# Optimization experiments

Hardware: AMD Instinct MI355X
Metric: run time of the kernel (lower is better)

The kernel has to match this reference:

```python
import jax, jax.numpy as jnp
import numpy as np

K = 16
EPS = 1e-5
SLOPE = 0.01  # nn.LeakyReLU default


def _bn(x, g, b):
    # BatchNorm1d in training mode applied to [N, C, k] in torch == normalize
    # per-channel over (N, k) axes of [N, k, C] here. Biased variance (ddof=0).
    m = x.mean(axis=(0, 1))
    v = x.var(axis=(0, 1))
    return (x - m) * jax.lax.rsqrt(v + EPS) * g + b


def _lrelu(x):
    return jnp.where(x >= 0, x, SLOPE * x)


def setup_inputs() -> dict:
    key = jax.random.key(0)
    ks = jax.random.split(key, 24)
    N, CIN, COUT = 8192, 256, 256
    s = 0.05
    inp = {
        "fea_i": jax.random.normal(ks[0], (N, CIN), jnp.float32),
        "fea_last": jax.random.normal(ks[1], (N, CIN), jnp.float32),
        "xyz_i": jax.random.uniform(ks[2], (N, 3), jnp.float32),
        "xyz_last": jax.random.uniform(ks[3], (N, 3), jnp.float32),
        "t_i": jnp.float32(2.0),
        "t_last": jnp.float32(1.0),
        # lin_p: Linear(4,64) -> BN(64) -> LeakyReLU -> Linear(64,COUT)
        "wp1": jax.random.normal(ks[4], (4, 64), jnp.float32) * s,
        "bp1": jnp.zeros((64,), jnp.float32),
        "gp": jnp.ones((64,), jnp.float32),
        "bp": jnp.zeros((64,), jnp.float32),
        "wp2": jax.random.normal(ks[5], (64, COUT), jnp.float32) * s,
        "bp2": jnp.zeros((COUT,), jnp.float32),
        # lin_q / lin_k / lin_v
        "wq": jax.random.normal(ks[6], (CIN, COUT), jnp.float32) * s,
        "bq": jnp.zeros((COUT,), jnp.float32),
        "wk": jax.random.normal(ks[7], (CIN, COUT), jnp.float32) * s,
        "bk": jnp.zeros((COUT,), jnp.float32),
        "wv": jax.random.normal(ks[8], (CIN, COUT), jnp.float32) * s,
        "bv": jnp.zeros((COUT,), jnp.float32),
        # lin_w: BN -> LeakyReLU -> Linear(COUT,COUT) -> BN -> LeakyReLU
        "gw1": jnp.ones((COUT,), jnp.float32),
        "bw1": jnp.zeros((COUT,), jnp.float32),
        "ww": jax.random.normal(ks[9], (COUT, COUT), jnp.float32) * s,
        "bw": jnp.zeros((COUT,), jnp.float32),
        "gw2": jnp.ones((COUT,), jnp.float32),
        "bw2": jnp.zeros((COUT,), jnp.float32),
    }
    return inp


def reference(fea_i, fea_last, xyz_i, xyz_last, t_i, t_last,
              wp1, bp1, gp, bp, wp2, bp2,
              wq, bq, wk, bk, wv, bv,
              gw1, bw1, ww, bw, gw2, bw2):
    # k-NN: for each query point in xyz_last, K nearest points in xyz_i
    d2 = (jnp.sum(xyz_last * xyz_last, -1)[:, None]
          + jnp.sum(xyz_i * xyz_i, -1)[None, :]
          - 2.0 * xyz_last @ xyz_i.T)              # [N, N]
    idx = jax.lax.top_k(-d2, K)[1]                 # [N, K] neighbor idx into xyz_i

    fi = fea_i[idx]                                # [N, K, CIN]
    xi = xyz_i[idx]                                # [N, K, 3]
    # pe = xyzt_i - xyzt_last ; the gathered "last" side is the query point itself
    pe = jnp.concatenate([xi - xyz_last[:, None, :],
                          (t_i - t_last) * jnp.ones_like(xi[..., :1])], axis=-1)  # [N,K,4]
    pe = pe @ wp1 + bp1
    pe = _lrelu(_bn(pe, gp, bp))
    pe = pe @ wp2 + bp2                            # [N, K, COUT]

    q = fea_last @ wq + bq                         # [N, COUT], broadcast over K
    w = q[:, None, :] - (fi @ wk + bk) + pe        # [N, K, COUT]
    w = _lrelu(_bn(w, gw1, bw1))
    w = w @ ww + bw
    w = _lrelu(_bn(w, gw2, bw2))
    w = jax.nn.softmax(w, axis=1)                  # softmax over K neighbors

    v = fi @ wv + bv + pe                          # [N, K, COUT]
    return jnp.sum(w * v, axis=1)                  # [N, COUT]
```

## Files before the change

kernel.cpp:

```cpp
#include <hip/hip_runtime.h>
#include <hip/hip_bf16.h>
#include <math.h>

#define N     8192
#define KNN   16
#define NK    (N*KNN)
#define C     256
#define CH    64
#define EPS   1e-5f
#define SLOPE 0.01f
#define LISTMAX 512

typedef __hip_bfloat16 bf16;
typedef short bfrag __attribute__((ext_vector_type(8)));
typedef float ffrag __attribute__((ext_vector_type(4)));

__device__ __forceinline__ float b2f(bf16 x){ return __bfloat162float(x); }
__device__ __forceinline__ bf16  f2b(float x){ return __float2bfloat16(x); }
__device__ __forceinline__ float b2fu(unsigned short s){
    return __uint_as_float(((unsigned)s) << 16);
}
__device__ __forceinline__ unsigned short f2bu(float x){
    union { bf16 h; unsigned short s; } u; u.h = f2b(x); return u.s;
}

union BF8 { unsigned short s[8]; uint4 u; };

template<typename T> __device__ __forceinline__ float ldv(const void* p, int i);
template<> __device__ __forceinline__ float ldv<float>(const void* p, int i){
    return ((const float*)p)[i];
}
template<> __device__ __forceinline__ float ldv<bf16>(const void* p, int i){
    return __bfloat162float(((const bf16*)p)[i]);
}
__device__ __forceinline__ bool is_f32(const void* ti){
    return ((const unsigned short*)ti)[0] == 0;
}

template<typename T>
__device__ __forceinline__ void stage8(const void* src, size_t off,
                                       unsigned short* dst){
    if (sizeof(T) == 4){
        const float4* s = (const float4*)((const float*)src + off);
        float4 a = s[0], b = s[1];
        BF8 o;
        o.s[0]=f2bu(a.x); o.s[1]=f2bu(a.y); o.s[2]=f2bu(a.z); o.s[3]=f2bu(a.w);
        o.s[4]=f2bu(b.x); o.s[5]=f2bu(b.y); o.s[6]=f2bu(b.z); o.s[7]=f2bu(b.w);
        *(uint4*)dst = o.u;
    } else {
        *(uint4*)dst = *(const uint4*)((const unsigned short*)src + off);
    }
}

__device__ __forceinline__ int mbcnt64(unsigned long long b){
    return __builtin_amdgcn_mbcnt_hi((unsigned)(b>>32),
           __builtin_amdgcn_mbcnt_lo((unsigned)b, 0));
}
__device__ __forceinline__ unsigned d2key(float d2){
    unsigned u = __float_as_uint(d2);
    return u ^ (((unsigned)(((int)u) >> 31)) | 0x80000000u);
}

__device__ __align__(256) int    g_idx[NK];
__device__ __align__(256) float  g_S[4096];
__device__ __align__(256) float  g_Rep[4*64*256];
__device__ __align__(256) float  g_M2[2048*9];
__device__ __align__(256) float4 g_pts[N];
__device__ __align__(256) int    g_cellCnt[4096];
__device__ __align__(256) int    g_cellStart[4100];
__device__ __align__(256) int    g_cellCur[4096];
__device__ __align__(256) float4 g_spts[N];
__device__ __align__(256) int    g_sidx[N];
__device__ __align__(256) unsigned short g_qT [C*C];
__device__ __align__(256) unsigned short g_kT [C*C];
__device__ __align__(256) unsigned short g_vT [C*C];
__device__ __align__(256) unsigned short g_wwT[C*C];
__device__ __align__(256) unsigned short g_p2T[C*CH];
__device__ __align__(256) unsigned short g_q  [N*C];
__device__ __align__(256) unsigned short g_fkb[N*C];
__device__ __align__(256) unsigned short g_fvb[N*C];
__device__ __align__(256) bf16   g_w1[NK*C];
__device__ __align__(256) bf16   g_vv[NK*C];
__device__ __align__(256) bf16   g_w2[NK*C];

__device__ __forceinline__ int cell_of(float4 c){
    int cx = (int)(c.x*16.f); cx = cx<0?0:(cx>15?15:cx);
    int cy = (int)(c.y*16.f); cy = cy<0?0:(cy>15?15:cy);
    int cz = (int)(c.z*16.f); cz = cz<0?0:(cz>15?15:cz);
    return (cz<<8) | (cy<<4) | cx;
}

__global__ __launch_bounds__(256) void kprepall(const void* xyz_i,
        const void* wq, const void* wk, const void* wv, const void* ww,
        const void* wp2, const void* ti_){
#pragma clang fp contract(off)
    const int b = blockIdx.x, tid = threadIdx.x;
    const bool f = is_f32(ti_);
    if (b < 64){
        int i = b*256 + tid;
        #pragma unroll
        for (int k = 0; k < 4; k++) g_Rep[i*4 + k] = 0.f;
        if (b < 16) g_S[i] = 0.f;
        else if (b < 32) g_cellCnt[(b-16)*256 + tid] = 0;
    } else if (b < 96){
        int p = (b-64)*256 + tid;
        float x = f ? ldv<float>(xyz_i, p*3+0) : ldv<bf16>(xyz_i, p*3+0);
        float y = f ? ldv<float>(xyz_i, p*3+1) : ldv<bf16>(xyz_i, p*3+1);
        float z = f ? ldv<float>(xyz_i, p*3+2) : ldv<bf16>(xyz_i, p*3+2);
        g_pts[p] = make_float4(x, y, z, (x*x + y*y) + z*z);
    } else {
        const void* src; unsigned short* dst; int K; int i0;
        if      (b <  352){ src=wq;  dst=g_qT;  K=256; i0=(b-  96)*256; }
        else if (b <  608){ src=wk;  dst=g_kT;  K=256; i0=(b- 352)*256; }
        else if (b <  864){ src=wv;  dst=g_vT;  K=256; i0=(b- 608)*256; }
        else if (b < 1120){ src=ww;  dst=g_wwT; K=256; i0=(b- 864)*256; }
        else              { src=wp2; dst=g_p2T; K=64;  i0=(b-1120)*256; }
        int i = i0 + tid;
        int k = i >> 8, n = i & 255;
        float v = f ? ldv<float>(src, i) : ldv<bf16>(src, i);
        dst[n*K + k] = f2bu(v);
    }
}

__global__ __launch_bounds__(256) void khist(){
    int p = blockIdx.x*256 + threadIdx.x;
    atomicAdd(&g_cellCnt[cell_of(g_pts[p])], 1);
}
__global__ __launch_bounds__(256) void kscan(){
    __shared__ int sc[256];
    const int tid = threadIdx.x;
    int carry = 0;
    for (int ch = 0; ch < 16; ch++){
        int i = ch*256 + tid;
        int v = g_cellCnt[i];
        sc[tid] = v;
        __syncthreads();
        for (int s = 1; s < 256; s <<= 1){
            int t_ = (tid >= s) ? sc[tid - s] : 0;
            __syncthreads();
            sc[tid] += t_;
            __syncthreads();
        }
        int excl = carry + sc[tid] - v;
        g_cellStart[i] = excl;
        g_cellCur[i]   = excl;
        carry += sc[255];
        __syncthreads();
    }
    if (tid == 0) g_cellStart[4096] = carry;
}
__global__ __launch_bounds__(256) void kscatter(){
    int p = blockIdx.x*256 + threadIdx.x;
    float4 c = g_pts[p];
    int pos = atomicAdd(&g_cellCur[cell_of(c)], 1);
    g_spts[pos] = c;
    g_sidx[pos] = p;
}

template<int D>
__device__ unsigned sel16(float qx, float qy, float qz, float sq, int lane){
#pragma clang fp contract(off)
    unsigned kk[D];
    #pragma unroll
    for (int i = 0; i < D; i++) kk[i] = 0xFFFFFFFFu;
    for (int t = 0; t < N/64; t++){
        float4 c = g_pts[t*64 + lane];
        float dot = (qx*c.x + qy*c.y) + qz*c.z;
        float d2  = (sq + c.w) - 2.0f*dot;
        unsigned u = d2key(d2);
        #pragma unroll
        for (int j = D-1; j > 0; --j){
            unsigned hi = (kk[j-1] > u) ? kk[j-1] : u;
            kk[j] = (kk[j] < hi) ? kk[j] : hi;
        }
        kk[0] = (kk[0] < u) ? kk[0] : u;
    }
    unsigned v16 = 0;
    for (int it = 0; it < 16; ++it){
        unsigned m = kk[0];
        #pragma unroll
        for (int s = 1; s < 64; s <<= 1){
            unsigned o = (unsigned)__shfl_xor((int)m, s, 64);
            m = (m < o) ? m : o;
        }
        unsigned long long ball = __ballot(kk[0] == m);
        int w = __ffsll(ball) - 1;
        if (lane == w){
            #pragma unroll
            for (int j = 0; j < D-1; j++) kk[j] = kk[j+1];
            kk[D-1] = 0xFFFFFFFFu;
        }
        v16 = m;
    }
    return v16;
}

__device__ int2 scan16(float qx, float qy, float qz, float sq, unsigned v16,
                       int lane, int* sure, int* tie){
#pragma clang fp contract(off)
    int nsure = 0, ntie = 0;
    for (int t = 0; t < N/64; t++){
        const int p = t*64 + lane;
        float4 c = g_pts[p];
        float dot = (qx*c.x + qy*c.y) + qz*c.z;
        float d2  = (sq + c.w) - 2.0f*dot;
        unsigned u = d2key(d2);
        bool bs = (u < v16), bt = (u == v16);
        unsigned long long Bs = __ballot(bs);
        unsigned long long Bt = __ballot(bt);
        if (bs){
            int pos = nsure + mbcnt64(Bs);
            if (pos < 16) sure[pos] = p;
        }
        if (bt){
            int pos = ntie + mbcnt64(Bt);
            if (pos < 16) tie[pos] = p;
        }
        nsure += (int)__popcll(Bs);
        ntie  += (int)__popcll(Bt);
    }
    return make_int2(nsure, ntie);
}

template<typename T>
__device__ void kknn_body(const void* xyz_last, int* sureL, int* tieL,
                          int* listL, float* momL){
#pragma clang fp contract(off)
    const int lane  = threadIdx.x & 63;
    const int wslot = threadIdx.x >> 6;
    const int q     = (blockIdx.x*256 + threadIdx.x) >> 6;
    const float qx = ldv<T>(xyz_last, q*3+0);
    const float qy = ldv<T>(xyz_last, q*3+1);
    const float qz = ldv<T>(xyz_last, q*3+2);
    const float sq = (qx*qx + qy*qy) + qz*qz;
    int* sure = &sureL[wslot*16];
    int* tie  = &tieL [wslot*16];
    int* list = &listL[wslot*LISTMAX];

    int cqx = (int)(qx*16.f); cqx = cqx<0?0:(cqx>15?15:cqx);
    int cqy = (int)(qy*16.f); cqy = cqy<0?0:(cqy>15?15:cqy);
    int cqz = (int)(qz*16.f); cqz = cqz<0?0:(cqz>15?15:cqz);

    int cnt0 = 0, cnt1 = 0, cs0 = 0, cs1 = 0;
    #pragma unroll
    for (int h = 0; h < 2; h++){
        int idx = lane*2 + h;
        if (idx < 125){
            int iz = idx/25, r = idx - iz*25, iy = r/5, ix = r - iy*5;
            int cx = cqx+ix-2, cy = cqy+iy-2, cz = cqz+iz-2;
            if ((unsigned)cx < 16u && (unsigned)cy < 16u && (unsigned)cz < 16u){
                int cell = (cz<<8) | (cy<<4) | cx;
                int s = g_cellStart[cell], e = g_cellStart[cell+1];
                if (h == 0){ cs0 = s; cnt0 = e - s; }
                else       { cs1 = s; cnt1 = e - s; }
            }
        }
    }
    int tot = cnt0 + cnt1;
    int incl = tot;
    #pragma unroll
    for (int s = 1; s < 64; s <<= 1){
        int u = __shfl_up(incl, s, 64);
        if (lane >= s) incl += u;
    }
    const int Tn = __shfl(incl, 63, 64);
    int base = incl - tot;
    bool full = (Tn > LISTMAX) || (Tn < 16);
    unsigned v16 = 0;
    int nsure = 0, ntie = 0;
    if (!full){
        for (int i = 0; i < cnt0; i++) list[base+i] = cs0 + i;
        for (int i = 0; i < cnt1; i++) list[base+cnt0+i] = cs1 + i;
        unsigned kk[4] = {~0u,~0u,~0u,~0u};
        int chunks = (Tn + 63) >> 6;
        for (int t = 0; t < chunks; t++){
            int li = t*64 + lane;
            unsigned u = 0xFFFFFFFFu;
            if (li < Tn){
                float4 c = g_spts[list[li]];
                float dot = (qx*c.x + qy*c.y) + qz*c.z;
                u = d2key((sq + c.w) - 2.0f*dot);
            }
            #pragma unroll
            for (int j = 3; j > 0; --j){
                unsigned hi = (kk[j-1] > u) ? kk[j-1] : u;
                kk[j] = (kk[j] < hi) ? kk[j] : hi;
            }
            kk[0] = (kk[0] < u) ? kk[0] : u;
        }
        for (int it = 0; it < 16; ++it){
            unsigned m = kk[0];
            #pragma unroll
            for (int s = 1; s < 64; s <<= 1){
                unsigned o = (unsigned)__shfl_xor((int)m, s, 64);
                m = (m < o) ? m : o;
            }
            unsigned long long ball = __ballot(kk[0] == m);
            int w = __ffsll(ball) - 1;
            if (lane == w){
                kk[0]=kk[1]; kk[1]=kk[2]; kk[2]=kk[3]; kk[3]=0xFFFFFFFFu;
            }
            v16 = m;
        }
        const float h_ = 0.0625f;
        float dmin = 1e30f;
        if (cqx-2 > 0)  dmin = fminf(dmin, qx - (float)(cqx-2)*h_);
        if (cqx+3 < 16) dmin = fminf(dmin, (float)(cqx+3)*h_ - qx);
        if (cqy-2 > 0)  dmin = fminf(dmin, qy - (float)(cqy-2)*h_);
        if (cqy+3 < 16) dmin = fminf(dmin, (float)(cqy+3)*h_ - qy);
        if (cqz-2 > 0)  dmin = fminf(dmin, qz - (float)(cqz-2)*h_);
        if (cqz+3 < 16) dmin = fminf(dmin, (float)(cqz+3)*h_ - qz);
        unsigned ub = d2key(dmin*dmin);
        if (!(v16 < ub)) full = true;
    }
    if (!full){
        int chunks = (Tn + 63) >> 6;
        for (int t = 0; t < chunks; t++){
            int li = t*64 + lane;
            unsigned u = 0xFFFFFFFFu; int oi = 0;
            if (li < Tn){
                int pos = list[li];
                float4 c = g_spts[pos];
                oi = g_sidx[pos];
                float dot = (qx*c.x + qy*c.y) + qz*c.z;
                u = d2key((sq + c.w) - 2.0f*dot);
            }
            bool bs = (li < Tn) && (u < v16);
            bool bt = (li < Tn) && (u == v16);
            unsigned long long Bs = __ballot(bs);
            unsigned long long Bt = __ballot(bt);
            if (bs){
                int pos2 = nsure + mbcnt64(Bs);
                if (pos2 < 16) sure[pos2] = oi;
            }
            if (bt){
                int pos2 = ntie + mbcnt64(Bt);
                if (pos2 < 16) tie[pos2] = oi;
            }
            nsure += (int)__popcll(Bs);
            ntie  += (int)__popcll(Bt);
        }
        if (nsure > 16 || (ntie > 16 && nsure < 16)) full = true;
    }
    const bool gridok = !full;
    if (full){
        v16 = sel16<16>(qx, qy, qz, sq, lane);
        int2 c2 = scan16(qx, qy, qz, sq, v16, lane, sure, tie);
        nsure = c2.x; ntie = c2.y;
    }
    if (nsure > 16) nsure = 16;
    int vsel = 0;
    if (lane < 16 && lane < nsure) vsel = sure[lane];
    if (gridok){
        int tv = (lane < (ntie < 16 ? ntie : 16)) ? tie[lane] : 0x7FFFFFFF;
        #pragma unroll
        for (int k = 2; k <= 16; k <<= 1)
            #pragma unroll
            for (int j = k>>1; j > 0; j >>= 1){
                int o = __shfl_xor(tv, j, 64);
                bool asc = ((lane & k) == 0);
                bool low = ((lane & j) == 0);
                int mn = tv < o ? tv : o;
                int mx = tv < o ? o : tv;
                tv = (asc == low) ? mn : mx;
            }
        int tfrom = __shfl(tv, (lane - nsure) & 63, 64);
        if (lane < 16 && lane >= nsure) vsel = tfrom;
    } else {
        if (lane < 16 && lane >= nsure) vsel = tie[lane - nsure];
    }
    float dx = 0.f, dy = 0.f, dz = 0.f;
    if (lane < 16){
        if ((unsigned)vsel >= (unsigned)N) vsel = 0;
        g_idx[q*KNN + lane] = vsel;
        float4 c = g_pts[vsel];
        dx = c.x - qx; dy = c.y - qy; dz = c.z - qz;
    }
    float mm[9] = {dx, dy, dz, dx*dx, dx*dy, dx*dz, dy*dy, dy*dz, dz*dz};
    #pragma unroll
    for (int j = 0; j < 9; j++){
        #pragma unroll
        for (int s = 1; s < 16; s <<= 1)
            mm[j] += __shfl_xor(mm[j], s, 64);
    }
    if (lane == 0){
        #pragma unroll
        for (int j = 0; j < 9; j++) momL[wslot*9 + j] = mm[j];
    }
    __syncthreads();
    if (threadIdx.x < 9){
        int t = threadIdx.x;
        g_M2[blockIdx.x*9 + t] = momL[t] + momL[9+t] + momL[18+t] + momL[27+t];
    }
}
__global__ __launch_bounds__(256) void kknn(const void* xyz_last, const void* ti_){
    __shared__ int sureL[4*16];
    __shared__ int tieL [4*16];
    __shared__ int listL[4*LISTMAX];
    __shared__ float momL[4*9];
    if (is_f32(ti_)) kknn_body<float>(xyz_last, sureL, tieL, listL, momL);
    else             kknn_body<bf16 >(xyz_last, sureL, tieL, listL, momL);
}

template<typename T>
__device__ void kgemm3m_body(const void* A, const unsigned short* BT,
                             const void* bias, unsigned short* out,
                             unsigned short* Al, unsigned short* Bl){
    const int tid  = threadIdx.x;
    const int c0   = blockIdx.x*128, r0 = blockIdx.y*128;
    const int lane = tid & 63, wv = tid >> 6;
    const int m    = lane & 15, qd = lane >> 4;
    const int rw   = (wv >> 1)*64, cw = (wv & 1)*64;
    ffrag acc[4][4];
    #pragma unroll
    for (int i = 0; i < 4; i++)
        #pragma unroll
        for (int j = 0; j < 4; j++)
            #pragma unroll
            for (int r = 0; r < 4; r++) acc[i][j][r] = 0.f;
    const int arow = tid >> 2, ach = tid & 3;
    for (int kt = 0; kt < 8; ++kt){
        __syncthreads();
        #pragma unroll
        for (int p = 0; p < 2; ++p){
            int row = arow + p*64;
            stage8<T>(A, (size_t)(r0+row)*C + kt*32 + ach*8, &Al[row*40 + ach*8]);
            *(uint4*)&Bl[row*40 + ach*8] =
                *(const uint4*)&BT[(c0+row)*C + kt*32 + ach*8];
        }
        __syncthreads();
        bfrag af[4], bfr[4];
        #pragma unroll
        for (int i = 0; i < 4; i++)
            af[i] = *(const bfrag*)&Al[(rw + i*16 + m)*40 + qd*8];
        #pragma unroll
        for (int j = 0; j < 4; j++)
            bfr[j] = *(const bfrag*)&Bl[(cw + j*16 + m)*40 + qd*8];
        #pragma unroll
        for (int i = 0; i < 4; i++)
            #pragma unroll
            for (int j = 0; j < 4; j++)
                acc[i][j] = __builtin_amdgcn_mfma_f32_16x16x32_bf16(
                                af[i], bfr[j], acc[i][j], 0, 0, 0);
    }
    float b4[4];
    #pragma unroll
    for (int j = 0; j < 4; j++) b4[j] = ldv<T>(bias, c0 + cw + j*16 + m);
    #pragma unroll
    for (int i = 0; i < 4; i++){
        #pragma unroll
        for (int r = 0; r < 4; r++){
            int row = r0 + rw + i*16 + qd*4 + r;
            unsigned short* orow = &out[(size_t)row*C];
            #pragma unroll
            for (int j = 0; j < 4; j++)
                orow[c0 + cw + j*16 + m] = f2bu(acc[i][j][r] + b4[j]);
        }
    }
}
__global__ __launch_bounds__(256) void kgemm3m(const void* fea_i, const void* fea_last,
        const void* bq, const void* bk, const void* bv, const void* ti_){
    __shared__ unsigned short Al[128*40];
    __shared__ unsigned short Bl[128*40];
    const int which = blockIdx.z;
    const void* A = (which==0) ? fea_last : fea_i;
    const unsigned short* BT = (which==0) ? g_qT : (which==1) ? g_kT : g_vT;
    const void* bias = (which==0) ? bq : (which==1) ? bk : bv;
    unsigned short* out = (which==0) ? g_q : (which==1) ? g_fkb : g_fvb;
    if (is_f32(ti_)) kgemm3m_body<float>(A, BT, bias, out, Al, Bl);
    else             kgemm3m_body<bf16 >(A, BT, bias, out, Al, Bl);
}

template<typename T>
__device__ void kfinpe_body(const void* wp1, const void* bp1,
                            const void* gp, const void* bp_,
                            const void* t_i, const void* t_last,
                            float* mTot, float* wred){
    const int tid = threadIdx.x, lane = tid & 63, wv = tid >> 6;
    float p[9];
    #pragma unroll
    for (int j = 0; j < 9; j++) p[j] = 0.f;
    for (int i = tid; i < 2048; i += 256){
        const float* m = &g_M2[i*9];
        #pragma unroll
        for (int j = 0; j < 9; j++) p[j] += m[j];
    }
    #pragma unroll
    for (int j = 0; j < 9; j++){
        #pragma unroll
        for (int s = 1; s < 64; s <<= 1) p[j] += __shfl_xor(p[j], s, 64);
    }
    if (lane == 0){
        #pragma unroll
        for (int j = 0; j < 9; j++) wred[wv*9 + j] = p[j];
    }
    __syncthreads();
    if (tid < 9) mTot[tid] = wred[tid] + wred[9+tid] + wred[18+tid] + wred[27+tid];
    __syncthreads();
    if (tid >= 64) return;
    const int c = tid;
    float M[9];
    #pragma unroll
    for (int j = 0; j < 9; j++) M[j] = mTot[j];
    const float w0 = ldv<T>(wp1, c),     w1 = ldv<T>(wp1, 64+c);
    const float w2 = ldv<T>(wp1, 128+c), w3 = ldv<T>(wp1, 192+c);
    const float dt = ldv<T>(t_i, 0) - ldv<T>(t_last, 0);
    const float be = dt*w3 + ldv<T>(bp1, c);
    const float NKf = (float)NK;
    float lin  = w0*M[0] + w1*M[1] + w2*M[2];
    float quad = w0*w0*M[3] + w1*w1*M[6] + w2*w2*M[8]
               + 2.f*(w0*w1*M[4] + w0*w2*M[5] + w1*w2*M[7]);
    float mean = (lin + NKf*be) / NKf;
    float ev2  = (quad + 2.f*be*lin + NKf*be*be) / NKf;
    float var  = ev2 - mean*mean;
    float sc   = ldv<T>(gp, c) * rsqrtf(var + EPS);
    g_S[128+c] = sc;
    g_S[192+c] = ldv<T>(bp_, c) - mean*sc;
}
__global__ void kfinpe(const void* wp1, const void* bp1, const void* gp,
                       const void* bp_, const void* t_i, const void* t_last){
    __shared__ float mTot[9];
    __shared__ float wred[4*9];
    if (is_f32(t_i)) kfinpe_body<float>(wp1, bp1, gp, bp_, t_i, t_last, mTot, wred);
    else             kfinpe_body<bf16 >(wp1, bp1, gp, bp_, t_i, t_last, mTot, wred);
}

__global__ void kfinalize(int Cn, int outOff, const void* g, const void* b,
                          const void* ti_, int repA){
    int c = threadIdx.x;
    if (c >= Cn) return;
    float s = 0.f, ss = 0.f;
    for (int r = 0; r < 64; r++){
        s  += g_Rep[((repA  )*64 + r)*256 + c];
        ss += g_Rep[((repA+1)*64 + r)*256 + c];
    }
    bool f = is_f32(ti_);
    float mean = s / (float)NK;
    float var  = ss / (float)NK - mean*mean;
    float gv = f ? ldv<float>(g, c) : ldv<bf16>(g, c);
    float bv = f ? ldv<float>(b, c) : ldv<bf16>(b, c);
    float sc = gv * rsqrtf(var + EPS);
    g_S[outOff+c]    = sc;
    g_S[outOff+Cn+c] = bv - mean*sc;
}

#define PE_LDP 68
template<typename T>
__device__ void kpe2m_body(const void* xyz_i, const void* xyz_last,
                           const void* wp1, const void* bp1, const void* bp2,
                           const void* t_i, const void* t_last,
                           unsigned short* Apel, unsigned short* Bpl,
                           float* peL, int* gl, float* s1w, float* s2w){
    const int tid  = threadIdx.x;
    const int lane = tid & 63, wv = tid >> 6;
    const int m    = lane & 15, qd = lane >> 4;
    const int rw   = (wv >> 1)*64, cw = (wv & 1)*64;
    const int c0   = blockIdx.x*128, r0 = blockIdx.y*128;
    if (tid < 128) gl[tid] = g_idx[r0 + tid];
    { int row = tid >> 1, half = tid & 1;
      #pragma unroll
      for (int e = 0; e < 4; e++)
          *(uint4*)&Bpl[row*72 + half*32 + e*8] =
              *(const uint4*)&g_p2T[(c0+row)*CH + half*32 + e*8];
    }
    __syncthreads();
    { const int kp = lane;
      const float w0 = ldv<T>(wp1, kp),     w1 = ldv<T>(wp1, 64+kp);
      const float w2 = ldv<T>(wp1, 128+kp), w3 = ldv<T>(wp1, 192+kp);
      const float b0 = ldv<T>(bp1, kp);
      const float sc = g_S[128+kp], sh = g_S[128+64+kp];
      const float dt = ldv<T>(t_i, 0) - ldv<T>(t_last, 0);
      #pragma unroll 4
      for (int p = 0; p < 32; p++){
          int row = wv*32 + p;
          int R = r0 + row; int n = R >> 4; int g = gl[row];
          float dx = ldv<T>(xyz_i, g*3+0) - ldv<T>(xyz_last, n*3+0);
          float dy = ldv<T>(xyz_i, g*3+1) - ldv<T>(xyz_last, n*3+1);
          float dz = ldv<T>(xyz_i, g*3+2) - ldv<T>(xyz_last, n*3+2);
          float v = dx*w0 + dy*w1 + dz*w2 + dt*w3 + b0;
          v = v*sc + sh;
          v = (v >= 0.f) ? v : SLOPE*v;
          Apel[row*72 + kp] = f2bu(v);
      } }
    __syncthreads();
    ffrag acc[4][4];
    #pragma unroll
    for (int i = 0; i < 4; i++)
        #pragma unroll
        for (int j = 0; j < 4; j++)
            #pragma unroll
            for (int r = 0; r < 4; r++) acc[i][j][r] = 0.f;
    #pragma unroll
    for (int ks = 0; ks < 2; ++ks){
        bfrag af[4], bfr[4];
        #pragma unroll
        for (int i = 0; i < 4; i++)
            af[i] = *(const bfrag*)&Apel[(rw + i*16 + m)*72 + ks*32 + qd*8];
        #pragma unroll
        for (int j = 0; j < 4; j++)
            bfr[j] = *(const bfrag*)&Bpl[(cw + j*16 + m)*72 + ks*32 + qd*8];
        #pragma unroll
        for (int i = 0; i < 4; i++)
            #pragma unroll
            for (int j = 0; j < 4; j++)
                acc[i][j] = __builtin_amdgcn_mfma_f32_16x16x32_bf16(
                                af[i], bfr[j], acc[i][j], 0, 0, 0);
    }
    float bp2v[4];
    #pragma unroll
    for (int j = 0; j < 4; j++) bp2v[j] = ldv<T>(bp2, c0 + cw + j*16 + m);
    #pragma unroll
    for (int i = 0; i < 4; i++)
        #pragma unroll
        for (int j = 0; j < 4; j++)
            #pragma unroll
            for (int r = 0; r < 4; r++) acc[i][j][r] += bp2v[j];

    const int rep = blockIdx.y & 63;
    const int cg  = tid & 7;
    const int rg  = tid >> 3;
    for (int h = 0; h < 2; ++h){
        __syncthreads();
        if ((wv & 1) == h){
            #pragma unroll
            for (int i = 0; i < 4; i++)
                #pragma unroll
                for (int j = 0; j < 4; j++)
                    #pragma unroll
                    for (int r = 0; r < 4; r++)
                        peL[(rw + i*16 + qd*4 + r)*PE_LDP + j*16 + m]
                            = acc[i][j][r];
        }
        __syncthreads();
        float cs8[8], cq8[8];
        #pragma unroll
        for (int e = 0; e < 8; e++){ cs8[e] = 0.f; cq8[e] = 0.f; }
        #pragma unroll
        for (int rr = 0; rr < 4; rr++){
            int row = rg*4 + rr;
            int R = r0 + row; int n = R >> 4; int g = gl[row];
            int colb = c0 + h*64 + cg*8;
            BF8 qb, kb, vb;
            qb.u = *(const uint4*)&g_q  [(size_t)n*C + colb];
            kb.u = *(const uint4*)&g_fkb[(size_t)g*C + colb];
            vb.u = *(const uint4*)&g_fvb[(size_t)g*C + colb];
            float4 p0 = *(const float4*)&peL[row*PE_LDP + cg*8];
            float4 p1 = *(const float4*)&peL[row*PE_LDP + cg*8 + 4];
            float pe8[8] = {p0.x,p0.y,p0.z,p0.w,p1.x,p1.y,p1.z,p1.w};
            BF8 w1o, vvo;
            #pragma unroll
            for (int e = 0; e < 8; e++){
                float pv = pe8[e];
                unsigned short bb = f2bu(b2fu(qb.s[e]) - b2fu(kb.s[e]) + pv);
                w1o.s[e] = bb;
                float rv = b2fu(bb);
                cs8[e] += rv; cq8[e] += rv*rv;
                vvo.s[e] = f2bu(b2fu(vb.s[e]) + pv);
            }
            *(uint4*)&((unsigned short*)g_w1)[(size_t)R*C + colb] = w1o.u;
            *(uint4*)&((unsigned short*)g_vv)[(size_t)R*C + colb] = vvo.u;
        }
        #pragma unroll
        for (int e = 0; e < 8; e++){
            #pragma unroll
            for (int s_ = 8; s_ < 64; s_ <<= 1){
                cs8[e] += __shfl_xor(cs8[e], s_, 64);
                cq8[e] += __shfl_xor(cq8[e], s_, 64);
            }
        }
        if (lane < 8){
            #pragma unroll
            for (int e = 0; e < 8; e++){
                s1w[wv*64 + lane*8 + e] = cs8[e];
                s2w[wv*64 + lane*8 + e] = cq8[e];
            }
        }
        __syncthreads();
        if (tid < 64){
            float a = s1w[tid] + s1w[64+tid] + s1w[128+tid] + s1w[192+tid];
            float b = s2w[tid] + s2w[64+tid] + s2w[128+tid] + s2w[192+tid];
            atomicAdd(&g_Rep[(0*64 + rep)*256 + c0 + h*64 + tid], a);
            atomicAdd(&g_Rep[(1*64 + rep)*256 + c0 + h*64 + tid], b);
        }
    }
}
__global__ __launch_bounds__(256) void kpe2m(const void* xyz_i, const void* xyz_last,
        const void* wp1, const void* bp1, const void* bp2,
        const void* t_i, const void* t_last){
    __shared__ __align__(16) unsigned char smem[128*72*2*2];
    __shared__ int gl[128];
    __shared__ float s1w[256], s2w[256];
    unsigned short* Apel = (unsigned short*)smem;
    unsigned short* Bpl  = Apel + 128*72;
    float* peL = (float*)smem;
    if (is_f32(t_i))
        kpe2m_body<float>(xyz_i, xyz_last, wp1, bp1, bp2, t_i, t_last,
                          Apel, Bpl, peL, gl, s1w, s2w);
    else
        kpe2m_body<bf16 >(xyz_i, xyz_last, wp1, bp1, bp2, t_i, t_last,
                          Apel, Bpl, peL, gl, s1w, s2w);
}

template<typename T>
__device__ void kgemmww_body(const void* bw, unsigned short* Al,
                             unsigned short* Bl, float* scl, float* shl,
                             float* t1w, float* t2w){
    const int tid  = threadIdx.x;
    const int c0   = blockIdx.x*128, r0 = blockIdx.y*128;
    const int lane = tid & 63, wv = tid >> 6;
    const int m    = lane & 15, qd = lane >> 4;
    const int rw   = (wv >> 1)*64, cw = (wv & 1)*64;
    scl[tid] = g_S[768 + tid]; shl[tid] = g_S[768 + C + tid];
    ffrag acc[4][4];
    #pragma unroll
    for (int i = 0; i < 4; i++)
        #pragma unroll
        for (int j = 0; j < 4; j++)
            #pragma unroll
            for (int r = 0; r < 4; r++) acc[i][j][r] = 0.f;
    const int arow = tid >> 2, ach = tid & 3;
    for (int kt = 0; kt < 8; ++kt){
        __syncthreads();
        #pragma unroll
        for (int p = 0; p < 2; ++p){
            int row = arow + p*64;
            int kk  = kt*32 + ach*8;
            BF8 in, o;
            in.u = *(const uint4*)&g_w1[(size_t)(r0+row)*C + kk];
            #pragma unroll
            for (int e = 0; e < 8; e++){
                float x = b2fu(in.s[e]);
                x = x*scl[kk+e] + shl[kk+e];
                x = (x >= 0.f) ? x : SLOPE*x;
                o.s[e] = f2bu(x);
            }
            *(uint4*)&Al[row*40 + ach*8] = o.u;
            *(uint4*)&Bl[row*40 + ach*8] =
                *(const uint4*)&g_wwT[(c0+row)*C + kt*32 + ach*8];
        }
        __syncthreads();
        bfrag af[4], bf_[4];
        #pragma unroll
        for (int i = 0; i < 4; i++)
            af[i] = *(const bfrag*)&Al[(rw + i*16 + m)*40 + qd*8];
        #pragma unroll
        for (int j = 0; j < 4; j++)
            bf_[j] = *(const bfrag*)&Bl[(cw + j*16 + m)*40 + qd*8];
        #pragma unroll
        for (int i = 0; i < 4; i++)
            #pragma unroll
            for (int j = 0; j < 4; j++)
                acc[i][j] = __builtin_amdgcn_mfma_f32_16x16x32_bf16(
                                af[i], bf_[j], acc[i][j], 0, 0, 0);
    }
    float bwv[4];
    #pragma unroll
    for (int j = 0; j < 4; j++) bwv[j] = ldv<T>(bw, c0 + cw + j*16 + m);
    float cs[4] = {0.f,0.f,0.f,0.f}, cq[4] = {0.f,0.f,0.f,0.f};
    #pragma unroll
    for (int j = 0; j < 4; j++){
        int col = c0 + cw + j*16 + m;
        #pragma unroll
        for (int i = 0; i < 4; i++){
            #pragma unroll
            for (int r = 0; r < 4; r++){
                int row = r0 + rw + i*16 + qd*4 + r;
                unsigned short bb = f2bu(acc[i][j][r] + bwv[j]);
                ((unsigned short*)g_w2)[(size_t)row*C + col] = bb;
                float rv = b2fu(bb);
                cs[j] += rv; cq[j] += rv*rv;
            }
        }
    }
    #pragma unroll
    for (int j = 0; j < 4; j++){
        cs[j] += __shfl_xor(cs[j], 16, 64); cs[j] += __shfl_xor(cs[j], 32, 64);
        cq[j] += __shfl_xor(cq[j], 16, 64); cq[j] += __shfl_xor(cq[j], 32, 64);
    }
    if (lane < 16){
        #pragma unroll
        for (int j = 0; j < 4; j++){
            t1w[(wv>>1)*128 + cw + j*16 + lane] = cs[j];
            t2w[(wv>>1)*128 + cw + j*16 + lane] = cq[j];
        }
    }
    __syncthreads();
    if (tid < 128){
        float a = t1w[tid] + t1w[128+tid];
        float b = t2w[tid] + t2w[128+tid];
        int rep = blockIdx.y & 63;
        atomicAdd(&g_Rep[(2*64 + rep)*256 + c0 + tid], a);
        atomicAdd(&g_Rep[(3*64 + rep)*256 + c0 + tid], b);
    }
}
__global__ __launch_bounds__(256) void kgemmww(const void* bw, const void* ti_){
    __shared__ unsigned short Al[128*40];
    __shared__ unsigned short Bl[128*40];
    __shared__ float scl[C], shl[C];
    __shared__ float t1w[256], t2w[256];
    if (is_f32(ti_)) kgemmww_body<float>(bw, Al, Bl, scl, shl, t1w, t2w);
    else             kgemmww_body<bf16 >(bw, Al, Bl, scl, shl, t1w, t2w);
}

__global__ __launch_bounds__(256) void kfinal(void* out, const void* ti_){
    const int n = blockIdx.x, c = threadIdx.x;
    const float sc = g_S[1792+c], sh = g_S[1792+C+c];
    float u[KNN];
    float m = -3.4e38f;
    #pragma unroll
    for (int k = 0; k < KNN; k++){
        float x = b2f(g_w2[(size_t)(n*KNN+k)*C + c])*sc + sh;
        x = (x >= 0.f) ? x : SLOPE*x;
        u[k] = x; m = fmaxf(m, x);
    }
    float ssum = 0.f, o = 0.f;
    #pragma unroll
    for (int k = 0; k < KNN; k++){
        float e = __expf(u[k] - m);
        ssum += e;
        o += e * b2f(g_vv[(size_t)(n*KNN+k)*C + c]);
    }
    float r = o / ssum;
    if (is_f32(ti_)) ((float*)out)[(size_t)n*C + c] = r;
    else             ((bf16*)out)[(size_t)n*C + c] = f2b(r);
}

extern "C" void kernel_launch(void* const* d_in, const int* in_sizes, int n_in,
                              void* d_out, int out_size, void* d_ws, size_t ws_size,
                              hipStream_t stream){
    const void* fea_i    = d_in[0];
    const void* fea_last = d_in[1];
    const void* xyz_i    = d_in[2];
    const void* xyz_last = d_in[3];
    const void* t_i      = d_in[4];
    const void* t_last   = d_in[5];
    const void* wp1 = d_in[6];
    const void* bp1 = d_in[7];
    const void* gp  = d_in[8];
    const void* bp_ = d_in[9];
    const void* wp2 = d_in[10];
    const void* bp2 = d_in[11];
    const void* wq  = d_in[12];
    const void* bq  = d_in[13];
    const void* wk  = d_in[14];
    const void* bk  = d_in[15];
    const void* wv  = d_in[16];
    const void* bv  = d_in[17];
    const void* gw1 = d_in[18];
    const void* bw1 = d_in[19];
    const void* ww  = d_in[20];
    const void* bw  = d_in[21];
    const void* gw2 = d_in[22];
    const void* bw2 = d_in[23];

    kprepall<<<1184, 256, 0, stream>>>(xyz_i, wq, wk, wv, ww, wp2, t_i);
    khist<<<32, 256, 0, stream>>>();
    kscan<<<1, 256, 0, stream>>>();
    kscatter<<<32, 256, 0, stream>>>();
    kknn<<<N/4, 256, 0, stream>>>(xyz_last, t_i);
    kgemm3m<<<dim3(2, 64, 3), 256, 0, stream>>>(fea_i, fea_last, bq, bk, bv, t_i);
    kfinpe<<<1, 256, 0, stream>>>(wp1, bp1, gp, bp_, t_i, t_last);
    kpe2m<<<dim3(2, NK/128), 256, 0, stream>>>(xyz_i, xyz_last, wp1, bp1, bp2,
                                               t_i, t_last);
    kfinalize<<<1, 256, 0, stream>>>(256, 768, gw1, bw1, t_i, 0);
    kgemmww<<<dim3(2, NK/128), 256, 0, stream>>>(bw, t_i);
    kfinalize<<<1, 256, 0, stream>>>(256, 1792, gw2, bw2, t_i, 2);
    kfinal<<<N, 256, 0, stream>>>(d_out, t_i);
}
```

Baseline: 313.1 us.

## Stage GEMM epilogue through LDS for coalesced stores and vectorize final loads

The ww GEMM epilogue now writes its bf16 outputs into shared memory, reusing the operand tile buffer, in two 64-column halves. It then emits 16-byte coalesced global stores and computes the BN column sums from the staged data with wave shuffles, replacing the scattered 2-byte stores. The final softmax kernel loads its 16x256 w2 and vv tiles with vector loads into padded LDS. The positional-encoding kernel reads precomputed float4 copies of the point coordinates instead of three scalar loads each. The trade is extra barriers and LDS traffic in the epilogue plus one more small prep pass over xyz_last.

```diff
diff --git a/kernel.cpp b/kernel.cpp
--- a/kernel.cpp
+++ b/kernel.cpp
@@ -66,6 +66,7 @@
 __device__ __align__(256) float  g_Rep[4*64*256];
 __device__ __align__(256) float  g_M2[2048*9];
 __device__ __align__(256) float4 g_pts[N];
+__device__ __align__(256) float4 g_qlast[N];
 __device__ __align__(256) int    g_cellCnt[4096];
 __device__ __align__(256) int    g_cellStart[4100];
 __device__ __align__(256) int    g_cellCur[4096];
@@ -91,6 +92,7 @@
 }
 
 __global__ __launch_bounds__(256) void kprepall(const void* xyz_i,
+        const void* xyz_last,
         const void* wq, const void* wk, const void* wv, const void* ww,
         const void* wp2, const void* ti_){
 #pragma clang fp contract(off)
@@ -108,13 +110,19 @@
         float y = f ? ldv<float>(xyz_i, p*3+1) : ldv<bf16>(xyz_i, p*3+1);
         float z = f ? ldv<float>(xyz_i, p*3+2) : ldv<bf16>(xyz_i, p*3+2);
         g_pts[p] = make_float4(x, y, z, (x*x + y*y) + z*z);
+    } else if (b < 128){
+        int p = (b-96)*256 + tid;
+        float x = f ? ldv<float>(xyz_last, p*3+0) : ldv<bf16>(xyz_last, p*3+0);
+        float y = f ? ldv<float>(xyz_last, p*3+1) : ldv<bf16>(xyz_last, p*3+1);
+        float z = f ? ldv<float>(xyz_last, p*3+2) : ldv<bf16>(xyz_last, p*3+2);
+        g_qlast[p] = make_float4(x, y, z, 0.f);
     } else {
         const void* src; unsigned short* dst; int K; int i0;
-        if      (b <  352){ src=wq;  dst=g_qT;  K=256; i0=(b-  96)*256; }
-        else if (b <  608){ src=wk;  dst=g_kT;  K=256; i0=(b- 352)*256; }
-        else if (b <  864){ src=wv;  dst=g_vT;  K=256; i0=(b- 608)*256; }
-        else if (b < 1120){ src=ww;  dst=g_wwT; K=256; i0=(b- 864)*256; }
-        else              { src=wp2; dst=g_p2T; K=64;  i0=(b-1120)*256; }
+        if      (b <  384){ src=wq;  dst=g_qT;  K=256; i0=(b- 128)*256; }
+        else if (b <  640){ src=wk;  dst=g_kT;  K=256; i0=(b- 384)*256; }
+        else if (b <  896){ src=wv;  dst=g_vT;  K=256; i0=(b- 640)*256; }
+        else if (b < 1152){ src=ww;  dst=g_wwT; K=256; i0=(b- 896)*256; }
+        else              { src=wp2; dst=g_p2T; K=64;  i0=(b-1152)*256; }
         int i = i0 + tid;
         int k = i >> 8, n = i & 255;
         float v = f ? ldv<float>(src, i) : ldv<bf16>(src, i);
@@ -574,9 +582,11 @@
       for (int p = 0; p < 32; p++){
           int row = wv*32 + p;
           int R = r0 + row; int n = R >> 4; int g = gl[row];
-          float dx = ldv<T>(xyz_i, g*3+0) - ldv<T>(xyz_last, n*3+0);
-          float dy = ldv<T>(xyz_i, g*3+1) - ldv<T>(xyz_last, n*3+1);
-          float dz = ldv<T>(xyz_i, g*3+2) - ldv<T>(xyz_last, n*3+2);
+          float4 cp = g_pts[g];
+          float4 qp = g_qlast[n];
+          float dx = cp.x - qp.x;
+          float dy = cp.y - qp.y;
+          float dz = cp.z - qp.z;
           float v = dx*w0 + dy*w1 + dz*w2 + dt*w3 + b0;
           v = v*sc + sh;
           v = (v >= 0.f) ? v : SLOPE*v;
@@ -703,8 +713,9 @@
 
 template<typename T>
 __device__ void kgemmww_body(const void* bw, unsigned short* Al,
-                             unsigned short* Bl, float* scl, float* shl,
-                             float* t1w, float* t2w){
+                             unsigned short* Bl, unsigned short* w2L,
+                             float* scl, float* shl,
+                             float* s1w, float* s2w){
     const int tid  = threadIdx.x;
     const int c0   = blockIdx.x*128, r0 = blockIdx.y*128;
     const int lane = tid & 63, wv = tid >> 6;
@@ -756,60 +767,101 @@
     float bwv[4];
     #pragma unroll
     for (int j = 0; j < 4; j++) bwv[j] = ldv<T>(bw, c0 + cw + j*16 + m);
-    float cs[4] = {0.f,0.f,0.f,0.f}, cq[4] = {0.f,0.f,0.f,0.f};
-    #pragma unroll
-    for (int j = 0; j < 4; j++){
-        int col = c0 + cw + j*16 + m;
-        #pragma unroll
-        for (int i = 0; i < 4; i++){
-            #pragma unroll
-            for (int r = 0; r < 4; r++){
-                int row = r0 + rw + i*16 + qd*4 + r;
-                unsigned short bb = f2bu(acc[i][j][r] + bwv[j]);
-                ((unsigned short*)g_w2)[(size_t)row*C + col] = bb;
-                float rv = b2fu(bb);
-                cs[j] += rv; cq[j] += rv*rv;
-            }
-        }
-    }
-    #pragma unroll
-    for (int j = 0; j < 4; j++){
-        cs[j] += __shfl_xor(cs[j], 16, 64); cs[j] += __shfl_xor(cs[j], 32, 64);
-        cq[j] += __shfl_xor(cq[j], 16, 64); cq[j] += __shfl_xor(cq[j], 32, 64);
-    }
-    if (lane < 16){
-        #pragma unroll
-        for (int j = 0; j < 4; j++){
-            t1w[(wv>>1)*128 + cw + j*16 + lane] = cs[j];
-            t2w[(wv>>1)*128 + cw + j*16 + lane] = cq[j];
-        }
+    #pragma unroll
+    for (int i = 0; i < 4; i++)
+        #pragma unroll
+        for (int j = 0; j < 4; j++)
+            #pragma unroll
+            for (int r = 0; r < 4; r++) acc[i][j][r] += bwv[j];
+
+    const int rep = blockIdx.y & 63;
+    const int cg  = tid & 7;
+    const int rg  = tid >> 3;
+    for (int h = 0; h < 2; ++h){
+        __syncthreads();
+        if ((wv & 1) == h){
+            #pragma unroll
+            for (int i = 0; i < 4; i++)
+                #pragma unroll
+                for (int j = 0; j < 4; j++)
+                    #pragma unroll
+                    for (int r = 0; r < 4; r++)
+                        w2L[(rw + i*16 + qd*4 + r)*72 + j*16 + m]
+                            = f2bu(acc[i][j][r]);
+        }
+        __syncthreads();
+        float cs8[8], cq8[8];
+        #pragma unroll
+        for (int e = 0; e < 8; e++){ cs8[e] = 0.f; cq8[e] = 0.f; }
+        #pragma unroll
+        for (int rr = 0; rr < 4; rr++){
+            int row = rg*4 + rr;
+            int colb = c0 + h*64 + cg*8;
+            BF8 o;
+            o.u = *(const uint4*)&w2L[row*72 + cg*8];
+            *(uint4*)&((unsigned short*)g_w2)[(size_t)(r0+row)*C + colb] = o.u;
+            #pragma unroll
+            for (int e = 0; e < 8; e++){
+                float rv = b2fu(o.s[e]);
+                cs8[e] += rv; cq8[e] += rv*rv;
+            }
+        }
+        #pragma unroll
+        for (int e = 0; e < 8; e++){
+            #pragma unroll
+            for (int s_ = 8; s_ < 64; s_ <<= 1){
+                cs8[e] += __shfl_xor(cs8[e], s_, 64);
+                cq8[e] += __shfl_xor(cq8[e], s_, 64);
+            }
+        }
+        if (lane < 8){
+            #pragma unroll
+            for (int e = 0; e < 8; e++){
+                s1w[wv*64 + lane*8 + e] = cs8[e];
+                s2w[wv*64 + lane*8 + e] = cq8[e];
+            }
+        }
+        __syncthreads();
+        if (tid < 64){
+            float a = s1w[tid] + s1w[64+tid] + s1w[128+tid] + s1w[192+tid];
+            float b = s2w[tid] + s2w[64+tid] + s2w[128+tid] + s2w[192+tid];
+            atomicAdd(&g_Rep[(2*64 + rep)*256 + c0 + h*64 + tid], a);
+            atomicAdd(&g_Rep[(3*64 + rep)*256 + c0 + h*64 + tid], b);
+        }
+    }
+}
+__global__ __launch_bounds__(256) void kgemmww(const void* bw, const void* ti_){
+    __shared__ __align__(16) unsigned char smem[128*40*2*2];
+    __shared__ float scl[C], shl[C];
+    __shared__ float s1w[256], s2w[256];
+    unsigned short* Al  = (unsigned short*)smem;
+    unsigned short* Bl  = Al + 128*40;
+    unsigned short* w2L = (unsigned short*)smem;
+    if (is_f32(ti_)) kgemmww_body<float>(bw, Al, Bl, w2L, scl, shl, s1w, s2w);
+    else             kgemmww_body<bf16 >(bw, Al, Bl, w2L, scl, shl, s1w, s2w);
+}
+
+__global__ __launch_bounds__(256) void kfinal(void* out, const void* ti_){
+    __shared__ unsigned short w2L[16*264];
+    __shared__ unsigned short vvL[16*264];
+    const int n = blockIdx.x, tid = threadIdx.x;
+    const unsigned short* w2g = (const unsigned short*)g_w2 + (size_t)n*KNN*C;
+    const unsigned short* vvg = (const unsigned short*)g_vv + (size_t)n*KNN*C;
+    #pragma unroll
+    for (int p = 0; p < 2; p++){
+        int off = p*2048 + tid*8;
+        int row = off >> 8, col = off & 255;
+        *(uint4*)&w2L[row*264 + col] = *(const uint4*)&w2g[off];
+        *(uint4*)&vvL[row*264 + col] = *(const uint4*)&vvg[off];
     }
     __syncthreads();
-    if (tid < 128){
-        float a = t1w[tid] + t1w[128+tid];
-        float b = t2w[tid] + t2w[128+tid];
-        int rep = blockIdx.y & 63;
-        atomicAdd(&g_Rep[(2*64 + rep)*256 + c0 + tid], a);
-        atomicAdd(&g_Rep[(3*64 + rep)*256 + c0 + tid], b);
-    }
-}
-__global__ __launch_bounds__(256) void kgemmww(const void* bw, const void* ti_){
-    __shared__ unsigned short Al[128*40];
-    __shared__ unsigned short Bl[128*40];
-    __shared__ float scl[C], shl[C];
-    __shared__ float t1w[256], t2w[256];
-    if (is_f32(ti_)) kgemmww_body<float>(bw, Al, Bl, scl, shl, t1w, t2w);
-    else             kgemmww_body<bf16 >(bw, Al, Bl, scl, shl, t1w, t2w);
-}
-
-__global__ __launch_bounds__(256) void kfinal(void* out, const void* ti_){
-    const int n = blockIdx.x, c = threadIdx.x;
+    const int c = tid;
     const float sc = g_S[1792+c], sh = g_S[1792+C+c];
     float u[KNN];
     float m = -3.4e38f;
     #pragma unroll
     for (int k = 0; k < KNN; k++){
-        float x = b2f(g_w2[(size_t)(n*KNN+k)*C + c])*sc + sh;
+        float x = b2fu(w2L[k*264 + c])*sc + sh;
         x = (x >= 0.f) ? x : SLOPE*x;
         u[k] = x; m = fmaxf(m, x);
     }
@@ -818,7 +870,7 @@
     for (int k = 0; k < KNN; k++){
         float e = __expf(u[k] - m);
         ssum += e;
-        o += e * b2f(g_vv[(size_t)(n*KNN+k)*C + c]);
+        o += e * b2fu(vvL[k*264 + c]);
     }
     float r = o / ssum;
     if (is_f32(ti_)) ((float*)out)[(size_t)n*C + c] = r;
@@ -853,7 +905,7 @@
     const void* gw2 = d_in[22];
     const void* bw2 = d_in[23];
 
-    kprepall<<<1184, 256, 0, stream>>>(xyz_i, wq, wk, wv, ww, wp2, t_i);
+    kprepall<<<1216, 256, 0, stream>>>(xyz_i, xyz_last, wq, wk, wv, ww, wp2, t_i);
     khist<<<32, 256, 0, stream>>>();
     kscan<<<1, 256, 0, stream>>>();
     kscatter<<<32, 256, 0, stream>>>();
```

After: 322.3 us. 1.03x slower.

## Merge kpe2m column tiles into one 512-thread block, stage kfinal via LDS

Applied to the files above, without the earlier changes.

kpe2m now uses 512-thread blocks that cover all 256 output columns of a 128-row tile. Previously two blocks each computed half the columns and both redid the gather, the PE first layer and the g_q/g_fkb loads. Query and candidate coordinates are precomputed as float4 arrays in kprepall, so the scattered 3-element loads become aligned vector loads. kfinal now stages its w2 and vv rows into shared memory with 16-byte loads, at the cost of more LDS use and lower occupancy per block.

```diff
diff --git a/kernel.cpp b/kernel.cpp
--- a/kernel.cpp
+++ b/kernel.cpp
@@ -66,6 +66,7 @@
 __device__ __align__(256) float  g_Rep[4*64*256];
 __device__ __align__(256) float  g_M2[2048*9];
 __device__ __align__(256) float4 g_pts[N];
+__device__ __align__(256) float4 g_qlast[N];
 __device__ __align__(256) int    g_cellCnt[4096];
 __device__ __align__(256) int    g_cellStart[4100];
 __device__ __align__(256) int    g_cellCur[4096];
@@ -91,6 +92,7 @@
 }
 
 __global__ __launch_bounds__(256) void kprepall(const void* xyz_i,
+        const void* xyz_last,
         const void* wq, const void* wk, const void* wv, const void* ww,
         const void* wp2, const void* ti_){
 #pragma clang fp contract(off)
@@ -108,13 +110,19 @@
         float y = f ? ldv<float>(xyz_i, p*3+1) : ldv<bf16>(xyz_i, p*3+1);
         float z = f ? ldv<float>(xyz_i, p*3+2) : ldv<bf16>(xyz_i, p*3+2);
         g_pts[p] = make_float4(x, y, z, (x*x + y*y) + z*z);
+    } else if (b < 128){
+        int p = (b-96)*256 + tid;
+        float x = f ? ldv<float>(xyz_last, p*3+0) : ldv<bf16>(xyz_last, p*3+0);
+        float y = f ? ldv<float>(xyz_last, p*3+1) : ldv<bf16>(xyz_last, p*3+1);
+        float z = f ? ldv<float>(xyz_last, p*3+2) : ldv<bf16>(xyz_last, p*3+2);
+        g_qlast[p] = make_float4(x, y, z, 0.f);
     } else {
         const void* src; unsigned short* dst; int K; int i0;
-        if      (b <  352){ src=wq;  dst=g_qT;  K=256; i0=(b-  96)*256; }
-        else if (b <  608){ src=wk;  dst=g_kT;  K=256; i0=(b- 352)*256; }
-        else if (b <  864){ src=wv;  dst=g_vT;  K=256; i0=(b- 608)*256; }
-        else if (b < 1120){ src=ww;  dst=g_wwT; K=256; i0=(b- 864)*256; }
-        else              { src=wp2; dst=g_p2T; K=64;  i0=(b-1120)*256; }
+        if      (b <  384){ src=wq;  dst=g_qT;  K=256; i0=(b- 128)*256; }
+        else if (b <  640){ src=wk;  dst=g_kT;  K=256; i0=(b- 384)*256; }
+        else if (b <  896){ src=wv;  dst=g_vT;  K=256; i0=(b- 640)*256; }
+        else if (b < 1152){ src=ww;  dst=g_wwT; K=256; i0=(b- 896)*256; }
+        else              { src=wp2; dst=g_p2T; K=64;  i0=(b-1152)*256; }
         int i = i0 + tid;
         int k = i >> 8, n = i & 255;
         float v = f ? ldv<float>(src, i) : ldv<bf16>(src, i);
@@ -544,24 +552,23 @@
     g_S[outOff+Cn+c] = bv - mean*sc;
 }
 
-#define PE_LDP 68
+#define PE_LDP 132
 template<typename T>
-__device__ void kpe2m_body(const void* xyz_i, const void* xyz_last,
-                           const void* wp1, const void* bp1, const void* bp2,
+__device__ void kpe2m_body(const void* wp1, const void* bp1, const void* bp2,
                            const void* t_i, const void* t_last,
                            unsigned short* Apel, unsigned short* Bpl,
                            float* peL, int* gl, float* s1w, float* s2w){
     const int tid  = threadIdx.x;
     const int lane = tid & 63, wv = tid >> 6;
     const int m    = lane & 15, qd = lane >> 4;
-    const int rw   = (wv >> 1)*64, cw = (wv & 1)*64;
-    const int c0   = blockIdx.x*128, r0 = blockIdx.y*128;
+    const int rw   = (wv >> 2)*64, cw = (wv & 3)*64;
+    const int r0   = blockIdx.x*128;
     if (tid < 128) gl[tid] = g_idx[r0 + tid];
     { int row = tid >> 1, half = tid & 1;
       #pragma unroll
       for (int e = 0; e < 4; e++)
           *(uint4*)&Bpl[row*72 + half*32 + e*8] =
-              *(const uint4*)&g_p2T[(c0+row)*CH + half*32 + e*8];
+              *(const uint4*)&g_p2T[row*CH + half*32 + e*8];
     }
     __syncthreads();
     { const int kp = lane;
@@ -571,12 +578,14 @@
       const float sc = g_S[128+kp], sh = g_S[128+64+kp];
       const float dt = ldv<T>(t_i, 0) - ldv<T>(t_last, 0);
       #pragma unroll 4
-      for (int p = 0; p < 32; p++){
-          int row = wv*32 + p;
+      for (int p = 0; p < 16; p++){
+          int row = wv*16 + p;
           int R = r0 + row; int n = R >> 4; int g = gl[row];
-          float dx = ldv<T>(xyz_i, g*3+0) - ldv<T>(xyz_last, n*3+0);
-          float dy = ldv<T>(xyz_i, g*3+1) - ldv<T>(xyz_last, n*3+1);
-          float dz = ldv<T>(xyz_i, g*3+2) - ldv<T>(xyz_last, n*3+2);
+          float4 cp = g_pts[g];
+          float4 qp = g_qlast[n];
+          float dx = cp.x - qp.x;
+          float dy = cp.y - qp.y;
+          float dz = cp.z - qp.z;
           float v = dx*w0 + dy*w1 + dz*w2 + dt*w3 + b0;
           v = v*sc + sh;
           v = (v >= 0.f) ? v : SLOPE*v;
@@ -608,7 +617,7 @@
     }
     float bp2v[4];
     #pragma unroll
-    for (int j = 0; j < 4; j++) bp2v[j] = ldv<T>(bp2, c0 + cw + j*16 + m);
+    for (int j = 0; j < 4; j++) bp2v[j] = ldv<T>(bp2, cw + j*16 + m);
     #pragma unroll
     for (int i = 0; i < 4; i++)
         #pragma unroll
@@ -616,19 +625,20 @@
             #pragma unroll
             for (int r = 0; r < 4; r++) acc[i][j][r] += bp2v[j];
 
-    const int rep = blockIdx.y & 63;
-    const int cg  = tid & 7;
-    const int rg  = tid >> 3;
+    const int rep = blockIdx.x & 63;
+    const int cg  = tid & 15;
+    const int rg  = tid >> 4;
     for (int h = 0; h < 2; ++h){
         __syncthreads();
-        if ((wv & 1) == h){
+        if (((wv >> 1) & 1) == h){
+            int lc0 = cw & 64;
             #pragma unroll
             for (int i = 0; i < 4; i++)
                 #pragma unroll
                 for (int j = 0; j < 4; j++)
                     #pragma unroll
                     for (int r = 0; r < 4; r++)
-                        peL[(rw + i*16 + qd*4 + r)*PE_LDP + j*16 + m]
+                        peL[(rw + i*16 + qd*4 + r)*PE_LDP + lc0 + j*16 + m]
                             = acc[i][j][r];
         }
         __syncthreads();
@@ -639,7 +649,7 @@
         for (int rr = 0; rr < 4; rr++){
             int row = rg*4 + rr;
             int R = r0 + row; int n = R >> 4; int g = gl[row];
-            int colb = c0 + h*64 + cg*8;
+            int colb = h*128 + cg*8;
             BF8 qb, kb, vb;
             qb.u = *(const uint4*)&g_q  [(size_t)n*C + colb];
             kb.u = *(const uint4*)&g_fkb[(size_t)g*C + colb];
@@ -662,43 +672,45 @@
         }
         #pragma unroll
         for (int e = 0; e < 8; e++){
-            #pragma unroll
-            for (int s_ = 8; s_ < 64; s_ <<= 1){
-                cs8[e] += __shfl_xor(cs8[e], s_, 64);
-                cq8[e] += __shfl_xor(cq8[e], s_, 64);
-            }
-        }
-        if (lane < 8){
+            cs8[e] += __shfl_xor(cs8[e], 16, 64);
+            cs8[e] += __shfl_xor(cs8[e], 32, 64);
+            cq8[e] += __shfl_xor(cq8[e], 16, 64);
+            cq8[e] += __shfl_xor(cq8[e], 32, 64);
+        }
+        if (lane < 16){
             #pragma unroll
             for (int e = 0; e < 8; e++){
-                s1w[wv*64 + lane*8 + e] = cs8[e];
-                s2w[wv*64 + lane*8 + e] = cq8[e];
+                s1w[wv*128 + lane*8 + e] = cs8[e];
+                s2w[wv*128 + lane*8 + e] = cq8[e];
             }
         }
         __syncthreads();
-        if (tid < 64){
-            float a = s1w[tid] + s1w[64+tid] + s1w[128+tid] + s1w[192+tid];
-            float b = s2w[tid] + s2w[64+tid] + s2w[128+tid] + s2w[192+tid];
-            atomicAdd(&g_Rep[(0*64 + rep)*256 + c0 + h*64 + tid], a);
-            atomicAdd(&g_Rep[(1*64 + rep)*256 + c0 + h*64 + tid], b);
-        }
-    }
-}
-__global__ __launch_bounds__(256) void kpe2m(const void* xyz_i, const void* xyz_last,
-        const void* wp1, const void* bp1, const void* bp2,
-        const void* t_i, const void* t_last){
-    __shared__ __align__(16) unsigned char smem[128*72*2*2];
+        if (tid < 128){
+            float a = 0.f, b = 0.f;
+            #pragma unroll
+            for (int w = 0; w < 8; w++){
+                a += s1w[w*128 + tid];
+                b += s2w[w*128 + tid];
+            }
+            atomicAdd(&g_Rep[(0*64 + rep)*256 + h*128 + tid], a);
+            atomicAdd(&g_Rep[(1*64 + rep)*256 + h*128 + tid], b);
+        }
+    }
+}
+__global__ __launch_bounds__(512) void kpe2m(const void* wp1, const void* bp1,
+        const void* bp2, const void* t_i, const void* t_last){
+    __shared__ __align__(16) unsigned char smem[128*PE_LDP*4];
     __shared__ int gl[128];
-    __shared__ float s1w[256], s2w[256];
+    __shared__ float s1w[8*128], s2w[8*128];
     unsigned short* Apel = (unsigned short*)smem;
     unsigned short* Bpl  = Apel + 128*72;
     float* peL = (float*)smem;
     if (is_f32(t_i))
-        kpe2m_body<float>(xyz_i, xyz_last, wp1, bp1, bp2, t_i, t_last,
-                          Apel, Bpl, peL, gl, s1w, s2w);
+        kpe2m_body<float>(wp1, bp1, bp2, t_i, t_last, Apel, Bpl, peL,
+                          gl, s1w, s2w);
     else
-        kpe2m_body<bf16 >(xyz_i, xyz_last, wp1, bp1, bp2, t_i, t_last,
-                          Apel, Bpl, peL, gl, s1w, s2w);
+        kpe2m_body<bf16 >(wp1, bp1, bp2, t_i, t_last, Apel, Bpl, peL,
+                          gl, s1w, s2w);
 }
 
 template<typename T>
@@ -803,13 +815,26 @@
 }
 
 __global__ __launch_bounds__(256) void kfinal(void* out, const void* ti_){
-    const int n = blockIdx.x, c = threadIdx.x;
+    __shared__ unsigned short w2L[16*264];
+    __shared__ unsigned short vvL[16*264];
+    const int n = blockIdx.x, tid = threadIdx.x;
+    const unsigned short* w2g = (const unsigned short*)g_w2 + (size_t)n*KNN*C;
+    const unsigned short* vvg = (const unsigned short*)g_vv + (size_t)n*KNN*C;
+    #pragma unroll
+    for (int p = 0; p < 2; p++){
+        int off = p*2048 + tid*8;
+        int row = off >> 8, col = off & 255;
+        *(uint4*)&w2L[row*264 + col] = *(const uint4*)&w2g[off];
+        *(uint4*)&vvL[row*264 + col] = *(const uint4*)&vvg[off];
+    }
+    __syncthreads();
+    const int c = tid;
     const float sc = g_S[1792+c], sh = g_S[1792+C+c];
     float u[KNN];
     float m = -3.4e38f;
     #pragma unroll
     for (int k = 0; k < KNN; k++){
-        float x = b2f(g_w2[(size_t)(n*KNN+k)*C + c])*sc + sh;
+        float x = b2fu(w2L[k*264 + c])*sc + sh;
         x = (x >= 0.f) ? x : SLOPE*x;
         u[k] = x; m = fmaxf(m, x);
     }
@@ -818,7 +843,7 @@
     for (int k = 0; k < KNN; k++){
         float e = __expf(u[k] - m);
         ssum += e;
-        o += e * b2f(g_vv[(size_t)(n*KNN+k)*C + c]);
+        o += e * b2fu(vvL[k*264 + c]);
     }
     float r = o / ssum;
     if (is_f32(ti_)) ((float*)out)[(size_t)n*C + c] = r;
@@ -853,15 +878,14 @@
     const void* gw2 = d_in[22];
     const void* bw2 = d_in[23];
 
-    kprepall<<<1184, 256, 0, stream>>>(xyz_i, wq, wk, wv, ww, wp2, t_i);
+    kprepall<<<1216, 256, 0, stream>>>(xyz_i, xyz_last, wq, wk, wv, ww, wp2, t_i);
     khist<<<32, 256, 0, stream>>>();
     kscan<<<1, 256, 0, stream>>>();
     kscatter<<<32, 256, 0, stream>>>();
     kknn<<<N/4, 256, 0, stream>>>(xyz_last, t_i);
     kgemm3m<<<dim3(2, 64, 3), 256, 0, stream>>>(fea_i, fea_last, bq, bk, bv, t_i);
     kfinpe<<<1, 256, 0, stream>>>(wp1, bp1, gp, bp_, t_i, t_last);
-    kpe2m<<<dim3(2, NK/128), 256, 0, stream>>>(xyz_i, xyz_last, wp1, bp1, bp2,
-                                               t_i, t_last);
+    kpe2m<<<dim3(NK/128), 512, 0, stream>>>(wp1, bp1, bp2, t_i, t_last);
     kfinalize<<<1, 256, 0, stream>>>(256, 768, gw1, bw1, t_i, 0);
     kgemmww<<<dim3(2, NK/128), 256, 0, stream>>>(bw, t_i);
     kfinalize<<<1, 256, 0, stream>>>(256, 1792, gw2, bw2, t_i, 2);
```

After: 325.1 us. 3.8% more time.
